# Optimization experiments

Measured on AMD Instinct MI355X. Metric: run time of the kernel, lower is better.

## Reference

```python
import jax, jax.numpy as jnp
import numpy as np

# Fixed architecture constants (match init_kwargs)
L = 4        # num_layers
E = 4        # embed_dim (forced: embedding rows are 4-bit patch vectors)
H = 512      # hidden_dim
NH = 8       # num_heads
HD = H // NH # head_dim = 64
FF = 1024    # feedforward_dim
S = 1024     # seq_len (num patches)
B = 4        # batch
NT = 17      # num_tokens (16 patterns + mask token)
MRP = 32     # max_relative_positions
EPS = 1e-5


def _layernorm(x, g, b):
    m = x.mean(-1, keepdims=True)
    v = x.var(-1, keepdims=True)  # torch LayerNorm uses biased variance
    return (x - m) / jnp.sqrt(v + EPS) * g + b


def setup_inputs() -> dict:
    key = jax.random.key(0)
    ks = jax.random.split(key, 16)
    patches = jax.random.randint(ks[0], (B, S), 0, 16)
    mask = jax.random.bernoulli(ks[1], 0.15, (B, S))
    # Frozen embedding table: rows 0..15 = binary 4-vectors, row 16 = all 2s (mask token)
    pat = np.array([[a, b, c, d] for a in range(2) for b in range(2)
                    for c in range(2) for d in range(2)], dtype=np.float32)
    emb = np.zeros((NT, E), np.float32)
    emb[:16] = pat
    emb[16] = 2.0
    emb_table = jnp.array(emb)

    def gn(k, shape, s=0.02):
        return jax.random.normal(k, shape, jnp.float32) * s

    return {
        'patches': patches,
        'mask': mask,
        'emb_table': emb_table,
        'Wi': gn(ks[2], (L, E, H)), 'bi': jnp.zeros((L, H)),
        'Wqkv': gn(ks[3], (L, H, 3 * H)), 'bqkv': jnp.zeros((L, 3 * H)),
        'Wo': gn(ks[4], (L, H, E)), 'bo': jnp.zeros((L, E)),
        'g1': jnp.ones((L, H)), 'b1n': jnp.zeros((L, H)),
        'Wf1': gn(ks[5], (L, E, FF)), 'bf1': jnp.zeros((L, FF)),
        'Wf2': gn(ks[6], (L, FF, E)), 'bf2': jnp.zeros((L, E)),
        'g2': jnp.ones((L, E)), 'b2n': jnp.zeros((L, E)),
        'relemb': jax.random.normal(ks[7], (L, 2 * MRP - 1, HD), jnp.float32),
        'Wout': gn(ks[8], (E, NT)), 'bout': jnp.zeros((NT,)),
    }


def reference(patches, mask, emb_table, Wi, bi, Wqkv, bqkv, Wo, bo,
              g1, b1n, Wf1, bf1, Wf2, bf2, g2, b2n, relemb, Wout, bout):
    # Embedding lookup + mask-token substitution
    x = emb_table[patches]                                # (B,S,E)
    x = jnp.where(mask[..., None], emb_table[-1], x)

    r = jnp.arange(S)
    relpos = jnp.clip(r[:, None] - r[None, :] + MRP - 1, 0, 2 * MRP - 2)  # (S,S)
    # The original's nested-loop mask-build reduces exactly to:
    #   score[b,q,k] += -inf  iff  mask[b,k] and q != k
    neg = jnp.where(mask[:, None, :] & (r[:, None] != r[None, :]),
                    -jnp.inf, 0.0)                        # (B,S,S)

    scale = 1.0 / np.sqrt(HD)
    for l in range(L):
        bias = relemb[l].sum(-1)[relpos]                  # (S,S) rel-pos bias
        xp = x @ Wi[l] + bi[l]                            # (B,S,H)
        xn = _layernorm(xp, g1[l], b1n[l])
        qkv = (xn @ Wqkv[l] + bqkv[l]).reshape(B, S, 3, NH, HD)
        q, k, v = qkv[:, :, 0], qkv[:, :, 1], qkv[:, :, 2]
        sc = jnp.einsum('bqhd,bkhd->bhqk', q, k) * scale + bias + neg[:, None]
        p = jax.nn.softmax(sc, axis=-1)                   # (B,NH,S,S)
        ao = jnp.einsum('bhqk,bkhd->bqhd', p, v).reshape(B, S, H)
        x = x + ao @ Wo[l] + bo[l]                        # residual 1 (embed dim E)
        ff = jax.nn.relu(_layernorm(x, g2[l], b2n[l]) @ Wf1[l] + bf1[l]) @ Wf2[l] + bf2[l]
        x = x + ff                                        # residual 2
    return x @ Wout + bout                                # (B,S,NT) logits
```

## Files before the change

### kernel.cpp

```cpp
#include <hip/hip_runtime.h>
#include <hip/hip_bf16.h>
#include <math.h>

#define B_ 4
#define S_ 1024
#define H_ 512
#define NH_ 8
#define HD_ 64
#define FF_ 1024
#define E_ 4
#define L_ 4
#define NT_ 17
#define BS_ 4096
#define EPS_ 1e-5f
#define L2E_ 1.4426950408889634f
#define SCL_ 0.18033688011112042f
#define KSPLIT_ 4

typedef __attribute__((ext_vector_type(8))) short short8;
typedef __attribute__((ext_vector_type(16))) float f32x16;
typedef float float4u __attribute__((ext_vector_type(4), aligned(4)));

__device__ inline ushort bf16_rne(float f) {
  unsigned u = __builtin_bit_cast(unsigned, f);
  u += 0x7FFFu + ((u >> 16) & 1u);
  return (ushort)(u >> 16);
}
__device__ inline unsigned pk_bf16(float a, float b) {
  return (unsigned)bf16_rne(a) | ((unsigned)bf16_rne(b) << 16);
}
__device__ inline unsigned pk2(float a, float b) {
  unsigned ua = __builtin_bit_cast(unsigned, a) + 0x8000u;
  unsigned ub = __builtin_bit_cast(unsigned, b) + 0x8000u;
  return __builtin_amdgcn_perm(ub, ua, 0x07060302u);
}
__device__ inline float ubf2f(ushort u) {
  return __builtin_bit_cast(float, ((unsigned)u) << 16);
}


__global__ __launch_bounds__(256) void k_init(const int* __restrict__ patches,
                                              const int* __restrict__ mask,
                                              const float* __restrict__ emb,
                                              const float* __restrict__ relemb,
                                              float* __restrict__ x,
                                              float* __restrict__ T,
                                              float* __restrict__ negT) {
  int gid = blockIdx.x * 256 + threadIdx.x;
  if (gid < BS_) {
    int mk = mask[gid];
    int row = mk ? (NT_ - 1) : patches[gid];
    ((float4*)x)[gid] = ((const float4*)emb)[row];
    negT[gid] = mk ? -1e30f : 0.f;
  } else {
    int idx = gid - BS_;
    if (idx < L_ * 2112) {
      int l = idx / 2112, j = idx - l * 2112;
      int c = 1086 - j;
      c = c < 0 ? 0 : (c > 62 ? 62 : c);
      const float* src = relemb + (size_t)(l * 63 + c) * 64;
      float s = 0.f;
#pragma unroll
      for (int d = 0; d < 64; d++) s += src[d];
      T[idx] = s * L2E_;
    }
  }
}

__global__ __launch_bounds__(256) void k_cvtw(const float* __restrict__ W,
                                              ushort* __restrict__ Wt) {
  __shared__ ushort Tr[64][72];
  int l = blockIdx.z, k0 = blockIdx.y * 64, n0 = blockIdx.x * 64;
  int t = threadIdx.x;
  const float* src = W + (size_t)l * 512 * 1536;
  int row = t >> 4, c4 = (t & 15) * 4;
#pragma unroll
  for (int rr = 0; rr < 4; rr++) {
    int k = rr * 16 + row;
    float4 v = *(const float4*)(src + (size_t)(k0 + k) * 1536 + n0 + c4);
    Tr[c4 + 0][k] = bf16_rne(v.x);
    Tr[c4 + 1][k] = bf16_rne(v.y);
    Tr[c4 + 2][k] = bf16_rne(v.z);
    Tr[c4 + 3][k] = bf16_rne(v.w);
  }
  __syncthreads();
  int nrow = t >> 2, kc = (t & 3) * 16;
  ushort* dst = Wt + ((size_t)(l * 1536 + n0 + nrow)) * 512 + k0 + kc;
  *(uint4*)dst = *(uint4*)&Tr[nrow][kc];
  *(uint4*)(dst + 8) = *(uint4*)&Tr[nrow][kc + 8];
}

__global__ __launch_bounds__(256) void k_inln(const float* __restrict__ x,
                                              const float* __restrict__ Wi,
                                              const float* __restrict__ bi,
                                              const float* __restrict__ g1,
                                              const float* __restrict__ b1n,
                                              ushort* __restrict__ xnbf) {
  __shared__ float red_s[4], red_q[4];
  int tok = blockIdx.x;
  int t = threadIdx.x;
  float4 xr = ((const float4*)x)[tok];
  int j0 = 2 * t, j1 = 2 * t + 1;
  float xp0 = bi[j0] + xr.x * Wi[j0] + xr.y * Wi[H_ + j0] + xr.z * Wi[2 * H_ + j0] + xr.w * Wi[3 * H_ + j0];
  float xp1 = bi[j1] + xr.x * Wi[j1] + xr.y * Wi[H_ + j1] + xr.z * Wi[2 * H_ + j1] + xr.w * Wi[3 * H_ + j1];
  float s = xp0 + xp1;
  float q = xp0 * xp0 + xp1 * xp1;
#pragma unroll
  for (int o = 32; o > 0; o >>= 1) {
    s += __shfl_xor(s, o);
    q += __shfl_xor(q, o);
  }
  int wid = t >> 6;
  if ((t & 63) == 0) { red_s[wid] = s; red_q[wid] = q; }
  __syncthreads();
  s = red_s[0] + red_s[1] + red_s[2] + red_s[3];
  q = red_q[0] + red_q[1] + red_q[2] + red_q[3];
  float mean = s * (1.f / (float)H_);
  float var = q * (1.f / (float)H_) - mean * mean;
  float rs = rsqrtf(var + EPS_);
  float v0 = (xp0 - mean) * rs * g1[j0] + b1n[j0];
  float v1 = (xp1 - mean) * rs * g1[j1] + b1n[j1];
  ((unsigned*)xnbf)[tok * 256 + t] = pk_bf16(v0, v1);
}

__global__ __launch_bounds__(256, 2) void k_qkv(const ushort* __restrict__ A,
                                                const ushort* __restrict__ Wt,
                                                const float* __restrict__ bias,
                                                ushort* __restrict__ qf,
                                                ushort* __restrict__ kf,
                                                ushort* __restrict__ vf) {
  __shared__ ushort At[2][128][72];
  __shared__ ushort Bt[2][128][72];
  int t = threadIdx.x;
  int n0 = blockIdx.x * 128, m0 = blockIdx.y * 128;
  bool tr = (n0 < 1024);
  int w = t >> 6, lq = t & 31, hh = (t >> 5) & 1;
  int wm = (w & 1) * 64, wn = (w >> 1) * 64;
  f32x16 acc[2][2];
#pragma unroll
  for (int mt = 0; mt < 2; mt++)
#pragma unroll
    for (int nt = 0; nt < 2; nt++)
#pragma unroll
      for (int i = 0; i < 16; i++) acc[mt][nt][i] = 0.f;

  uint4 ar[4], br[4];

#define QLOADREGS(k0_)                                                         \
  {                                                                            \
    _Pragma("unroll") for (int j = 0; j < 4; j++) {                            \
      int idl = 256 * j + t;                                                   \
      int row = idl >> 3, u = idl & 7;                                         \
      ar[j] = *(const uint4*)(A + (size_t)(m0 + row) * 512 + (k0_) + u * 8);   \
      br[j] = *(const uint4*)(Wt + (size_t)(n0 + row) * 512 + (k0_) + u * 8);  \
    }                                                                          \
  }
#define QWRITELDS(buf_)                                                        \
  {                                                                            \
    _Pragma("unroll") for (int j = 0; j < 4; j++) {                            \
      int idl = 256 * j + t;                                                   \
      int row = idl >> 3, u = idl & 7;                                         \
      *(uint4*)&At[buf_][row][u * 8] = ar[j];                                  \
      *(uint4*)&Bt[buf_][row][u * 8] = br[j];                                  \
    }                                                                          \
  }

  QLOADREGS(0);
  QWRITELDS(0);
  __syncthreads();

  for (int it = 0; it < 8; it++) {
    int buf = it & 1;
    if (it < 7) { QLOADREGS((it + 1) * 64); }
#pragma unroll
    for (int kc = 0; kc < 4; kc++) {
      short8 af[2], bf[2];
#pragma unroll
      for (int mt = 0; mt < 2; mt++) af[mt] = *(const short8*)&At[buf][wm + mt * 32 + lq][kc * 16 + hh * 8];
#pragma unroll
      for (int nt = 0; nt < 2; nt++) bf[nt] = *(const short8*)&Bt[buf][wn + nt * 32 + lq][kc * 16 + hh * 8];
#pragma unroll
      for (int mt = 0; mt < 2; mt++)
#pragma unroll
        for (int nt = 0; nt < 2; nt++) {
          if (tr)
            acc[mt][nt] = __builtin_amdgcn_mfma_f32_32x32x16_bf16(bf[nt], af[mt], acc[mt][nt], 0, 0, 0);
          else
            acc[mt][nt] = __builtin_amdgcn_mfma_f32_32x32x16_bf16(af[mt], bf[nt], acc[mt][nt], 0, 0, 0);
        }
    }
    if (it < 7) {
      QWRITELDS(buf ^ 1);
      __syncthreads();
    }
  }
#undef QLOADREGS
#undef QWRITELDS

  if (tr) {
#pragma unroll
    for (int mt = 0; mt < 2; mt++) {
      int token = m0 + wm + mt * 32 + lq;
      int bb = token >> 10, sr = token & 1023;
      int qt = sr >> 5, lqp = sr & 31;
#pragma unroll
      for (int nt = 0; nt < 2; nt++) {
        int nn = n0 + wn + nt * 32;
        int nloc = (nn < 512) ? nn : nn - 512;
        ushort* dst = (nn < 512) ? qf : kf;
        int hd = nloc >> 6;
        int bh = bb * 8 + hd;
        size_t fragbase = ((size_t)(bh * 32 + qt)) * 4 * 512;
#pragma unroll
        for (int rg = 0; rg < 4; rg++) {
          int nbase = nn + rg * 8 + hh * 4;
          float4 bv = *(const float4*)(bias + nbase);
          float v0 = acc[mt][nt][rg * 4 + 0] + bv.x;
          float v1 = acc[mt][nt][rg * 4 + 1] + bv.y;
          float v2 = acc[mt][nt][rg * 4 + 2] + bv.z;
          float v3 = acc[mt][nt][rg * 4 + 3] + bv.w;
          int d0 = (nloc & 63) + rg * 8 + hh * 4;
          size_t addr = fragbase + (size_t)(d0 >> 4) * 512 +
                        (size_t)(((d0 >> 3) & 1) * 32 + lqp) * 8 + (d0 & 7);
          *(uint2*)(dst + addr) = make_uint2(pk_bf16(v0, v1), pk_bf16(v2, v3));
        }
      }
    }
  } else {
#pragma unroll
    for (int nt = 0; nt < 2; nt++) {
      int n = n0 + wn + nt * 32 + lq;
      int nloc = n - 1024;
      int hd = nloc >> 6, d = nloc & 63;
      float bb_ = bias[n];
#pragma unroll
      for (int mt = 0; mt < 2; mt++) {
#pragma unroll
        for (int rg = 0; rg < 4; rg++) {
          int tb = m0 + wm + mt * 32 + rg * 8 + hh * 4;
          int bb = tb >> 10, sr = tb & 1023;
          int bh = bb * 8 + hd;
          float v0 = acc[mt][nt][rg * 4 + 0] + bb_;
          float v1 = acc[mt][nt][rg * 4 + 1] + bb_;
          float v2 = acc[mt][nt][rg * 4 + 2] + bb_;
          float v3 = acc[mt][nt][rg * 4 + 3] + bb_;
          size_t addr = ((size_t)((bh * 2 + (d >> 5)) * 64 + (sr >> 4))) * 512 +
                        (size_t)(((sr >> 3) & 1) * 32 + (d & 31)) * 8 + (sr & 7);
          *(uint2*)(vf + addr) = make_uint2(pk_bf16(v0, v1), pk_bf16(v2, v3));
        }
      }
    }
  }
}

__global__ __launch_bounds__(256, 3) void k_attn(const ushort* __restrict__ qf,
                                                 const ushort* __restrict__ kf,
                                                 const ushort* __restrict__ vf,
                                                 const float* __restrict__ Tl,
                                                 const float* __restrict__ negT,
                                                 const float* __restrict__ Wol,
                                                 float* __restrict__ AOp,
                                                 float* __restrict__ lpart) {
  __shared__ ushort Pt[4][32][72];
  int t = threadIdx.x;
  int w = t >> 6, lane = t & 63;
  int lq = lane & 31, hh = lane >> 5;
  int id = blockIdx.x;
  int bh = id & 31;
  int slot = id >> 5;
  int qtg = slot & 7, j = slot >> 3;
  int b = bh >> 3, head = bh & 7;
  int qt = qtg * 4 + w;
  int q = qt * 32 + lq;
  int kstart = j * 256;

  const ushort* qbase = qf + ((size_t)(bh * 32 + qt)) * 2048 + lane * 8;
  short8 Qf[4];
#pragma unroll
  for (int c = 0; c < 4; c++) Qf[c] = *(const short8*)(qbase + c * 512);

  float Tlo = Tl[1086];
  float Thi = Tl[1024];

  float l_run = 0.f;
  f32x16 Ot[2];
#pragma unroll
  for (int dt = 0; dt < 2; dt++)
#pragma unroll
    for (int i = 0; i < 16; i++) Ot[dt][i] = 0.f;

  for (int it = 0; it < 4; it++) {
    int k0 = kstart + it * 64;
    short8 Kb[2][4];
#pragma unroll
    for (int st = 0; st < 2; st++) {
      const ushort* kb = kf + ((size_t)(bh * 32 + (k0 >> 5) + st)) * 2048 + lane * 8;
#pragma unroll
      for (int c = 0; c < 4; c++) Kb[st][c] = *(const short8*)(kb + c * 512);
    }
    short8 Vb[2][4];
#pragma unroll
    for (int dt = 0; dt < 2; dt++) {
      const ushort* vb = vf + ((size_t)((bh * 2 + dt) * 64 + (k0 >> 4))) * 512 + lane * 8;
#pragma unroll
      for (int c = 0; c < 4; c++) Vb[dt][c] = *(const short8*)(vb + c * 512);
    }
    f32x16 sa[2];
#pragma unroll
    for (int st = 0; st < 2; st++) {
      f32x16 a;
#pragma unroll
      for (int i = 0; i < 16; i++) a[i] = 0.f;
#pragma unroll
      for (int c = 0; c < 4; c++)
        a = __builtin_amdgcn_mfma_f32_32x32x16_bf16(Kb[st][c], Qf[c], a, 0, 0, 0);
      sa[st] = a;
    }
#pragma unroll
    for (int st = 0; st < 2; st++) {
      int kt0 = k0 + st * 32;
      int delta = kt0 - qt * 32;
      if (delta >= 64 || delta <= -64) {
        float bconst = (delta >= 64) ? Tlo : Thi;
#pragma unroll
        for (int rg = 0; rg < 4; rg++) {
          int krun = kt0 + rg * 8 + hh * 4;
          float4 nv = *(const float4*)(negT + b * S_ + krun);
          float p0 = exp2f(fmaf(sa[st][rg * 4 + 0], SCL_, bconst + nv.x));
          float p1 = exp2f(fmaf(sa[st][rg * 4 + 1], SCL_, bconst + nv.y));
          float p2 = exp2f(fmaf(sa[st][rg * 4 + 2], SCL_, bconst + nv.z));
          float p3 = exp2f(fmaf(sa[st][rg * 4 + 3], SCL_, bconst + nv.w));
          l_run += (p0 + p1) + (p2 + p3);
          *(uint2*)&Pt[w][lq][st * 32 + rg * 8 + hh * 4] = make_uint2(pk2(p0, p1), pk2(p2, p3));
        }
      } else {
#pragma unroll
        for (int rg = 0; rg < 4; rg++) {
          int krun = kt0 + rg * 8 + hh * 4;
          float4u bv = *(const float4u*)(Tl + (krun - q + 31 + 1024));
          float4 nv = *(const float4*)(negT + b * S_ + krun);
          float p[4];
#pragma unroll
          for (int i = 0; i < 4; i++) {
            float nvi = (i == 0) ? nv.x : (i == 1) ? nv.y : (i == 2) ? nv.z : nv.w;
            float t0 = (krun + i == q) ? bv[i] : (bv[i] + nvi);
            p[i] = exp2f(fmaf(sa[st][rg * 4 + i], SCL_, t0));
            l_run += p[i];
          }
          *(uint2*)&Pt[w][lq][st * 32 + rg * 8 + hh * 4] = make_uint2(pk2(p[0], p[1]), pk2(p[2], p[3]));
        }
      }
    }
    short8 Pf[4];
#pragma unroll
    for (int c = 0; c < 4; c++) Pf[c] = *(const short8*)&Pt[w][lq][c * 16 + hh * 8];
#pragma unroll
    for (int dt = 0; dt < 2; dt++)
#pragma unroll
      for (int c = 0; c < 4; c++)
        Ot[dt] = __builtin_amdgcn_mfma_f32_32x32x16_bf16(Vb[dt][c], Pf[c], Ot[dt], 0, 0, 0);
  }
  const float* woh = Wol + head * 64 * 4;
  float pe0 = 0.f, pe1 = 0.f, pe2 = 0.f, pe3 = 0.f;
#pragma unroll
  for (int dt = 0; dt < 2; dt++)
#pragma unroll
    for (int rg = 0; rg < 4; rg++)
#pragma unroll
      for (int i = 0; i < 4; i++) {
        int d = dt * 32 + rg * 8 + hh * 4 + i;
        float4 wv = *(const float4*)(woh + d * 4);
        float o = Ot[dt][rg * 4 + i];
        pe0 = fmaf(o, wv.x, pe0);
        pe1 = fmaf(o, wv.y, pe1);
        pe2 = fmaf(o, wv.z, pe2);
        pe3 = fmaf(o, wv.w, pe3);
      }
  pe0 += __shfl_xor(pe0, 32);
  pe1 += __shfl_xor(pe1, 32);
  pe2 += __shfl_xor(pe2, 32);
  pe3 += __shfl_xor(pe3, 32);
  float l_tot = l_run + __shfl_xor(l_run, 32);
  if (hh == 0) {
    float* ao = AOp + (size_t)j * (BS_ * NH_ * 4) + ((size_t)(b * S_ + q) * NH_ + head) * 4;
    *(float4*)ao = make_float4(pe0, pe1, pe2, pe3);
    lpart[((size_t)j * 32 + bh) * S_ + q] = l_tot;
  }
}

__global__ __launch_bounds__(256) void k_resffn(const float* __restrict__ AOp,
                                                const float* __restrict__ lpart,
                                                const float* __restrict__ bo,
                                                const float* __restrict__ g2,
                                                const float* __restrict__ b2n,
                                                const float* __restrict__ Wf1,
                                                const float* __restrict__ bf1,
                                                const float* __restrict__ Wf2,
                                                const float* __restrict__ bf2,
                                                float* __restrict__ x,
                                                const float* __restrict__ Wi,
                                                const float* __restrict__ bi,
                                                const float* __restrict__ g1,
                                                const float* __restrict__ b1n,
                                                ushort* __restrict__ xnbf,
                                                int doinln,
                                                const float* __restrict__ Wout,
                                                const float* __restrict__ bout,
                                                float* __restrict__ out,
                                                int dofinal) {
  int tok = blockIdx.x * 4 + (threadIdx.x >> 6);
  int lane = threadIdx.x & 63;
  int b = tok >> 10, qq = tok & 1023;
  int h = lane & 7;
  int lidx = (b * 8 + h) * 1024 + qq;
  float ls = lpart[lidx] + lpart[lidx + 32768] + lpart[lidx + 65536] + lpart[lidx + 98304];
  float inv = 1.f / ls;
  size_t abase = ((size_t)tok * 8 + h) * 4;
  float4 v0 = *(const float4*)(AOp + abase);
  float4 v1 = *(const float4*)(AOp + abase + 131072);
  float4 v2 = *(const float4*)(AOp + abase + 262144);
  float4 v3 = *(const float4*)(AOp + abase + 393216);
  float r0 = (v0.x + v1.x + v2.x + v3.x) * inv;
  float r1 = (v0.y + v1.y + v2.y + v3.y) * inv;
  float r2 = (v0.z + v1.z + v2.z + v3.z) * inv;
  float r3 = (v0.w + v1.w + v2.w + v3.w) * inv;
#pragma unroll
  for (int o = 1; o < 8; o <<= 1) {
    r0 += __shfl_xor(r0, o); r1 += __shfl_xor(r1, o);
    r2 += __shfl_xor(r2, o); r3 += __shfl_xor(r3, o);
  }
  float4 xo = *(const float4*)&x[tok * 4];
  float x0 = xo.x + r0 + bo[0];
  float x1 = xo.y + r1 + bo[1];
  float x2 = xo.z + r2 + bo[2];
  float x3 = xo.w + r3 + bo[3];
  float mn = 0.25f * (x0 + x1 + x2 + x3);
  float d0 = x0 - mn, d1 = x1 - mn, d2 = x2 - mn, d3 = x3 - mn;
  float var = 0.25f * (d0 * d0 + d1 * d1 + d2 * d2 + d3 * d3);
  float rs = rsqrtf(var + EPS_);
  float l0 = d0 * rs * g2[0] + b2n[0];
  float l1 = d1 * rs * g2[1] + b2n[1];
  float l2 = d2 * rs * g2[2] + b2n[2];
  float l3 = d3 * rs * g2[3] + b2n[3];
  float f0 = 0, f1 = 0, f2 = 0, f3 = 0;
#pragma unroll
  for (int f4 = 0; f4 < FF_ / 64; f4++) {
    int f = lane + f4 * 64;
    float hh = bf1[f] + l0 * Wf1[f] + l1 * Wf1[FF_ + f] + l2 * Wf1[2 * FF_ + f] + l3 * Wf1[3 * FF_ + f];
    hh = fmaxf(hh, 0.f);
    float4 w2 = *(const float4*)&Wf2[f * 4];
    f0 += hh * w2.x; f1 += hh * w2.y; f2 += hh * w2.z; f3 += hh * w2.w;
  }
#pragma unroll
  for (int o = 1; o < 64; o <<= 1) {
    f0 += __shfl_xor(f0, o); f1 += __shfl_xor(f1, o);
    f2 += __shfl_xor(f2, o); f3 += __shfl_xor(f3, o);
  }
  x0 += f0 + bf2[0]; x1 += f1 + bf2[1]; x2 += f2 + bf2[2]; x3 += f3 + bf2[3];
  if (dofinal) {
    if (lane < NT_)
      out[tok * NT_ + lane] = bout[lane] + x0 * Wout[lane] + x1 * Wout[NT_ + lane] +
                              x2 * Wout[2 * NT_ + lane] + x3 * Wout[3 * NT_ + lane];
    return;
  }
  if (lane == 0) *(float4*)&x[tok * 4] = make_float4(x0, x1, x2, x3);
  if (doinln) {
    float xp[8];
    float s = 0.f, qs = 0.f;
#pragma unroll
    for (int k = 0; k < 8; k++) {
      int jj = 64 * k + lane;
      float v = bi[jj] + x0 * Wi[jj] + x1 * Wi[H_ + jj] + x2 * Wi[2 * H_ + jj] + x3 * Wi[3 * H_ + jj];
      xp[k] = v;
      s += v;
      qs += v * v;
    }
#pragma unroll
    for (int o = 1; o < 64; o <<= 1) {
      s += __shfl_xor(s, o);
      qs += __shfl_xor(qs, o);
    }
    float mean = s * (1.f / (float)H_);
    float var1 = qs * (1.f / (float)H_) - mean * mean;
    float rs1 = rsqrtf(var1 + EPS_);
#pragma unroll
    for (int k = 0; k < 8; k++) {
      int jj = 64 * k + lane;
      float v = (xp[k] - mean) * rs1 * g1[jj] + b1n[jj];
      xnbf[tok * H_ + jj] = bf16_rne(v);
    }
  }
}

extern "C" void kernel_launch(void* const* d_in, const int* in_sizes, int n_in,
                              void* d_out, int out_size, void* d_ws, size_t ws_size,
                              hipStream_t stream) {
  const int* patches = (const int*)d_in[0];
  const int* mask = (const int*)d_in[1];
  const float* emb = (const float*)d_in[2];
  const float* Wi = (const float*)d_in[3];
  const float* bi = (const float*)d_in[4];
  const float* Wqkv = (const float*)d_in[5];
  const float* bqkv = (const float*)d_in[6];
  const float* Wo = (const float*)d_in[7];
  const float* bo = (const float*)d_in[8];
  const float* g1 = (const float*)d_in[9];
  const float* b1n = (const float*)d_in[10];
  const float* Wf1 = (const float*)d_in[11];
  const float* bf1 = (const float*)d_in[12];
  const float* Wf2 = (const float*)d_in[13];
  const float* bf2 = (const float*)d_in[14];
  const float* g2 = (const float*)d_in[15];
  const float* b2n = (const float*)d_in[16];
  const float* relemb = (const float*)d_in[17];
  const float* Wout = (const float*)d_in[18];
  const float* bout = (const float*)d_in[19];
  float* out = (float*)d_out;

  char* p = (char*)d_ws;
  float* x = (float*)p;          p += (size_t)BS_ * 4 * 4;
  float* T = (float*)p;          p += (size_t)L_ * 2112 * 4;
  float* negT = (float*)p;       p += (size_t)BS_ * 4;
  float* AOp = (float*)p;        p += (size_t)KSPLIT_ * BS_ * NH_ * 4 * 4;
  float* lpart = (float*)p;      p += (size_t)KSPLIT_ * 32 * 1024 * 4;
  ushort* xnbf = (ushort*)p;     p += (size_t)BS_ * H_ * 2;
  ushort* Wt = (ushort*)p;       p += (size_t)L_ * 1536 * 512 * 2;
  ushort* qf = (ushort*)p;       p += (size_t)32 * 1024 * 64 * 2;
  ushort* kf = (ushort*)p;       p += (size_t)32 * 1024 * 64 * 2;
  ushort* vf = (ushort*)p;       p += (size_t)32 * 64 * 1024 * 2;

  k_init<<<dim3(49), dim3(256), 0, stream>>>(patches, mask, emb, relemb, x, T, negT);
  k_cvtw<<<dim3(24, 8, 4), dim3(256), 0, stream>>>(Wqkv, Wt);
  k_inln<<<dim3(BS_), dim3(256), 0, stream>>>(x, Wi, bi, g1, b1n, xnbf);
  for (int l = 0; l < L_; l++) {
    k_qkv<<<dim3(12, 32), dim3(256), 0, stream>>>(xnbf, Wt + (size_t)l * 1536 * 512,
                                                  bqkv + l * 3 * H_, qf, kf, vf);
    k_attn<<<dim3(1024), dim3(256), 0, stream>>>(qf, kf, vf, T + l * 2112, negT,
                                                 Wo + l * H_ * E_, AOp, lpart);
    int nl = l + 1;
    k_resffn<<<dim3(1024), dim3(256), 0, stream>>>(
        AOp, lpart, bo + l * E_, g2 + l * E_, b2n + l * E_,
        Wf1 + l * E_ * FF_, bf1 + l * FF_, Wf2 + l * FF_ * E_, bf2 + l * E_, x,
        Wi + nl * E_ * H_, bi + nl * H_, g1 + nl * H_, b1n + nl * H_, xnbf,
        (l < L_ - 1) ? 1 : 0, Wout, bout, out, (l == L_ - 1) ? 1 : 0);
  }
}
```

Measured before the change: 338.4 us.

## Fuse all layers into one persistent cooperative kernel with grid syncs

Replaces the separate init, weight-convert, input-layernorm, QKV, attention and residual/FFN launches with a single cooperative kernel of 256 blocks of 1024 threads, separated by grid.sync barriers. The QKV GEMM is re-tiled so each of 16 waves computes one 32x32 MFMA tile, and tiles are looped over the persistent blocks. The goal is to remove kernel launch overhead and inter-kernel gaps. In exchange it adds grid-wide barriers and lower occupancy from 1024-thread blocks with 72KB shared memory, and the QKV tile count (384) does not divide evenly over 256 blocks.

```diff
diff --git a/kernel.cpp b/kernel.cpp
--- a/kernel.cpp
+++ b/kernel.cpp
@@ -1,14 +1,15 @@
 #include <hip/hip_runtime.h>
+#include <hip/hip_cooperative_groups.h>
 #include <hip/hip_bf16.h>
 #include <math.h>
+
+namespace cg = cooperative_groups;
 
 #define B_ 4
 #define S_ 1024
 #define H_ 512
 #define NH_ 8
-#define HD_ 64
 #define FF_ 1024
-#define E_ 4
 #define L_ 4
 #define NT_ 17
 #define BS_ 4096
@@ -16,6 +17,7 @@
 #define L2E_ 1.4426950408889634f
 #define SCL_ 0.18033688011112042f
 #define KSPLIT_ 4
+#define SMEM_BYTES 73728
 
 typedef __attribute__((ext_vector_type(8))) short short8;
 typedef __attribute__((ext_vector_type(16))) float f32x16;
@@ -25,523 +27,440 @@
   unsigned u = __builtin_bit_cast(unsigned, f);
   u += 0x7FFFu + ((u >> 16) & 1u);
   return (ushort)(u >> 16);
-}
-__device__ inline unsigned pk_bf16(float a, float b) {
-  return (unsigned)bf16_rne(a) | ((unsigned)bf16_rne(b) << 16);
 }
 __device__ inline unsigned pk2(float a, float b) {
   unsigned ua = __builtin_bit_cast(unsigned, a) + 0x8000u;
   unsigned ub = __builtin_bit_cast(unsigned, b) + 0x8000u;
   return __builtin_amdgcn_perm(ub, ua, 0x07060302u);
 }
-__device__ inline float ubf2f(ushort u) {
-  return __builtin_bit_cast(float, ((unsigned)u) << 16);
-}
-
-
-__global__ __launch_bounds__(256) void k_init(const int* __restrict__ patches,
-                                              const int* __restrict__ mask,
-                                              const float* __restrict__ emb,
-                                              const float* __restrict__ relemb,
-                                              float* __restrict__ x,
-                                              float* __restrict__ T,
-                                              float* __restrict__ negT) {
-  int gid = blockIdx.x * 256 + threadIdx.x;
-  if (gid < BS_) {
-    int mk = mask[gid];
-    int row = mk ? (NT_ - 1) : patches[gid];
-    ((float4*)x)[gid] = ((const float4*)emb)[row];
-    negT[gid] = mk ? -1e30f : 0.f;
-  } else {
-    int idx = gid - BS_;
-    if (idx < L_ * 2112) {
-      int l = idx / 2112, j = idx - l * 2112;
-      int c = 1086 - j;
-      c = c < 0 ? 0 : (c > 62 ? 62 : c);
-      const float* src = relemb + (size_t)(l * 63 + c) * 64;
-      float s = 0.f;
-#pragma unroll
-      for (int d = 0; d < 64; d++) s += src[d];
-      T[idx] = s * L2E_;
+
+struct P_ {
+  const int *patches, *mask;
+  const float *emb, *Wi, *bi, *Wqkv, *bqkv, *Wo, *bo, *g1, *b1n;
+  const float *Wf1, *bf1, *Wf2, *bf2, *g2, *b2n, *relemb, *Wout, *bout;
+  float *out, *x, *T, *negT, *AOp, *lpart;
+  ushort *xnbf, *Wt, *qf, *kf, *vf;
+};
+
+__global__ __launch_bounds__(1024, 4) void k_all(P_ p) {
+  extern __shared__ char smem[];
+  cg::grid_group grid = cg::this_grid();
+  int bid = blockIdx.x, tid = threadIdx.x;
+  int w16 = tid >> 6, lane = tid & 63, lq = lane & 31, hh = lane >> 5;
+
+  {
+    int gid = bid * 1024 + tid;
+    if (gid < BS_) {
+      int mk = p.mask[gid];
+      int row = mk ? 16 : p.patches[gid];
+      ((float4*)p.x)[gid] = ((const float4*)p.emb)[row];
+      p.negT[gid] = mk ? -1e30f : 0.f;
+    } else {
+      int idx = gid - BS_;
+      if (idx < L_ * 2112) {
+        int l = idx / 2112, jj = idx - l * 2112;
+        int c = 1086 - jj;
+        c = c < 0 ? 0 : (c > 62 ? 62 : c);
+        const float* src = p.relemb + (size_t)(l * 63 + c) * 64;
+        float s = 0.f;
+#pragma unroll
+        for (int d = 0; d < 64; d++) s += src[d];
+        p.T[idx] = s * L2E_;
+      }
+    }
+    {
+      int token = bid * 16 + w16;
+      int mk = p.mask[token];
+      int row = mk ? 16 : p.patches[token];
+      float4 e = ((const float4*)p.emb)[row];
+      float xp[8];
+      float s = 0.f, qs = 0.f;
+#pragma unroll
+      for (int k = 0; k < 8; k++) {
+        int jj = 64 * k + lane;
+        float v = p.bi[jj] + e.x * p.Wi[jj] + e.y * p.Wi[512 + jj] +
+                  e.z * p.Wi[1024 + jj] + e.w * p.Wi[1536 + jj];
+        xp[k] = v; s += v; qs += v * v;
+      }
+#pragma unroll
+      for (int o = 1; o < 64; o <<= 1) { s += __shfl_xor(s, o); qs += __shfl_xor(qs, o); }
+      float mean = s * (1.f / 512.f);
+      float var = qs * (1.f / 512.f) - mean * mean;
+      float rs = rsqrtf(var + EPS_);
+#pragma unroll
+      for (int k = 0; k < 8; k++) {
+        int jj = 64 * k + lane;
+        p.xnbf[token * 512 + jj] = bf16_rne((xp[k] - mean) * rs * p.g1[jj] + p.b1n[jj]);
+      }
+    }
+    {
+      int q4 = tid >> 8, qtid = tid & 255;
+      int unit = bid * 4 + q4;
+      bool act = unit < 768;
+      ushort(*Tr)[72] = (ushort(*)[72])(smem + q4 * 64 * 72 * 2);
+      int l = unit / 192, rem = unit % 192;
+      int k0 = (rem / 24) * 64, n0 = (rem % 24) * 64;
+      if (act) {
+        const float* src = p.Wqkv + (size_t)l * 512 * 1536;
+        int row = qtid >> 4, c4 = (qtid & 15) * 4;
+#pragma unroll
+        for (int rr = 0; rr < 4; rr++) {
+          int k = rr * 16 + row;
+          float4 v = *(const float4*)(src + (size_t)(k0 + k) * 1536 + n0 + c4);
+          Tr[c4 + 0][k] = bf16_rne(v.x); Tr[c4 + 1][k] = bf16_rne(v.y);
+          Tr[c4 + 2][k] = bf16_rne(v.z); Tr[c4 + 3][k] = bf16_rne(v.w);
+        }
+      }
+      __syncthreads();
+      if (act) {
+        int nrow = qtid >> 2, kc = (qtid & 3) * 16;
+        ushort* dst = p.Wt + ((size_t)(l * 1536 + n0 + nrow)) * 512 + k0 + kc;
+        *(uint4*)dst = *(uint4*)&Tr[nrow][kc];
+        *(uint4*)(dst + 8) = *(uint4*)&Tr[nrow][kc + 8];
+      }
     }
   }
-}
-
-__global__ __launch_bounds__(256) void k_cvtw(const float* __restrict__ W,
-                                              ushort* __restrict__ Wt) {
-  __shared__ ushort Tr[64][72];
-  int l = blockIdx.z, k0 = blockIdx.y * 64, n0 = blockIdx.x * 64;
-  int t = threadIdx.x;
-  const float* src = W + (size_t)l * 512 * 1536;
-  int row = t >> 4, c4 = (t & 15) * 4;
-#pragma unroll
-  for (int rr = 0; rr < 4; rr++) {
-    int k = rr * 16 + row;
-    float4 v = *(const float4*)(src + (size_t)(k0 + k) * 1536 + n0 + c4);
-    Tr[c4 + 0][k] = bf16_rne(v.x);
-    Tr[c4 + 1][k] = bf16_rne(v.y);
-    Tr[c4 + 2][k] = bf16_rne(v.z);
-    Tr[c4 + 3][k] = bf16_rne(v.w);
-  }
-  __syncthreads();
-  int nrow = t >> 2, kc = (t & 3) * 16;
-  ushort* dst = Wt + ((size_t)(l * 1536 + n0 + nrow)) * 512 + k0 + kc;
-  *(uint4*)dst = *(uint4*)&Tr[nrow][kc];
-  *(uint4*)(dst + 8) = *(uint4*)&Tr[nrow][kc + 8];
-}
-
-__global__ __launch_bounds__(256) void k_inln(const float* __restrict__ x,
-                                              const float* __restrict__ Wi,
-                                              const float* __restrict__ bi,
-                                              const float* __restrict__ g1,
-                                              const float* __restrict__ b1n,
-                                              ushort* __restrict__ xnbf) {
-  __shared__ float red_s[4], red_q[4];
-  int tok = blockIdx.x;
-  int t = threadIdx.x;
-  float4 xr = ((const float4*)x)[tok];
-  int j0 = 2 * t, j1 = 2 * t + 1;
-  float xp0 = bi[j0] + xr.x * Wi[j0] + xr.y * Wi[H_ + j0] + xr.z * Wi[2 * H_ + j0] + xr.w * Wi[3 * H_ + j0];
-  float xp1 = bi[j1] + xr.x * Wi[j1] + xr.y * Wi[H_ + j1] + xr.z * Wi[2 * H_ + j1] + xr.w * Wi[3 * H_ + j1];
-  float s = xp0 + xp1;
-  float q = xp0 * xp0 + xp1 * xp1;
-#pragma unroll
-  for (int o = 32; o > 0; o >>= 1) {
-    s += __shfl_xor(s, o);
-    q += __shfl_xor(q, o);
-  }
-  int wid = t >> 6;
-  if ((t & 63) == 0) { red_s[wid] = s; red_q[wid] = q; }
-  __syncthreads();
-  s = red_s[0] + red_s[1] + red_s[2] + red_s[3];
-  q = red_q[0] + red_q[1] + red_q[2] + red_q[3];
-  float mean = s * (1.f / (float)H_);
-  float var = q * (1.f / (float)H_) - mean * mean;
-  float rs = rsqrtf(var + EPS_);
-  float v0 = (xp0 - mean) * rs * g1[j0] + b1n[j0];
-  float v1 = (xp1 - mean) * rs * g1[j1] + b1n[j1];
-  ((unsigned*)xnbf)[tok * 256 + t] = pk_bf16(v0, v1);
-}
-
-__global__ __launch_bounds__(256, 2) void k_qkv(const ushort* __restrict__ A,
-                                                const ushort* __restrict__ Wt,
-                                                const float* __restrict__ bias,
-                                                ushort* __restrict__ qf,
-                                                ushort* __restrict__ kf,
-                                                ushort* __restrict__ vf) {
-  __shared__ ushort At[2][128][72];
-  __shared__ ushort Bt[2][128][72];
-  int t = threadIdx.x;
-  int n0 = blockIdx.x * 128, m0 = blockIdx.y * 128;
-  bool tr = (n0 < 1024);
-  int w = t >> 6, lq = t & 31, hh = (t >> 5) & 1;
-  int wm = (w & 1) * 64, wn = (w >> 1) * 64;
-  f32x16 acc[2][2];
-#pragma unroll
-  for (int mt = 0; mt < 2; mt++)
-#pragma unroll
-    for (int nt = 0; nt < 2; nt++)
-#pragma unroll
-      for (int i = 0; i < 16; i++) acc[mt][nt][i] = 0.f;
-
-  uint4 ar[4], br[4];
-
-#define QLOADREGS(k0_)                                                         \
-  {                                                                            \
-    _Pragma("unroll") for (int j = 0; j < 4; j++) {                            \
-      int idl = 256 * j + t;                                                   \
-      int row = idl >> 3, u = idl & 7;                                         \
-      ar[j] = *(const uint4*)(A + (size_t)(m0 + row) * 512 + (k0_) + u * 8);   \
-      br[j] = *(const uint4*)(Wt + (size_t)(n0 + row) * 512 + (k0_) + u * 8);  \
-    }                                                                          \
-  }
-#define QWRITELDS(buf_)                                                        \
-  {                                                                            \
-    _Pragma("unroll") for (int j = 0; j < 4; j++) {                            \
-      int idl = 256 * j + t;                                                   \
-      int row = idl >> 3, u = idl & 7;                                         \
-      *(uint4*)&At[buf_][row][u * 8] = ar[j];                                  \
-      *(uint4*)&Bt[buf_][row][u * 8] = br[j];                                  \
-    }                                                                          \
-  }
-
-  QLOADREGS(0);
-  QWRITELDS(0);
-  __syncthreads();
-
-  for (int it = 0; it < 8; it++) {
-    int buf = it & 1;
-    if (it < 7) { QLOADREGS((it + 1) * 64); }
-#pragma unroll
-    for (int kc = 0; kc < 4; kc++) {
-      short8 af[2], bf[2];
-#pragma unroll
-      for (int mt = 0; mt < 2; mt++) af[mt] = *(const short8*)&At[buf][wm + mt * 32 + lq][kc * 16 + hh * 8];
-#pragma unroll
-      for (int nt = 0; nt < 2; nt++) bf[nt] = *(const short8*)&Bt[buf][wn + nt * 32 + lq][kc * 16 + hh * 8];
-#pragma unroll
-      for (int mt = 0; mt < 2; mt++)
-#pragma unroll
-        for (int nt = 0; nt < 2; nt++) {
-          if (tr)
-            acc[mt][nt] = __builtin_amdgcn_mfma_f32_32x32x16_bf16(bf[nt], af[mt], acc[mt][nt], 0, 0, 0);
-          else
-            acc[mt][nt] = __builtin_amdgcn_mfma_f32_32x32x16_bf16(af[mt], bf[nt], acc[mt][nt], 0, 0, 0);
-        }
-    }
-    if (it < 7) {
-      QWRITELDS(buf ^ 1);
-      __syncthreads();
-    }
-  }
-#undef QLOADREGS
-#undef QWRITELDS
-
-  if (tr) {
-#pragma unroll
-    for (int mt = 0; mt < 2; mt++) {
-      int token = m0 + wm + mt * 32 + lq;
-      int bb = token >> 10, sr = token & 1023;
-      int qt = sr >> 5, lqp = sr & 31;
-#pragma unroll
-      for (int nt = 0; nt < 2; nt++) {
-        int nn = n0 + wn + nt * 32;
-        int nloc = (nn < 512) ? nn : nn - 512;
-        ushort* dst = (nn < 512) ? qf : kf;
-        int hd = nloc >> 6;
-        int bh = bb * 8 + hd;
-        size_t fragbase = ((size_t)(bh * 32 + qt)) * 4 * 512;
-#pragma unroll
-        for (int rg = 0; rg < 4; rg++) {
-          int nbase = nn + rg * 8 + hh * 4;
-          float4 bv = *(const float4*)(bias + nbase);
-          float v0 = acc[mt][nt][rg * 4 + 0] + bv.x;
-          float v1 = acc[mt][nt][rg * 4 + 1] + bv.y;
-          float v2 = acc[mt][nt][rg * 4 + 2] + bv.z;
-          float v3 = acc[mt][nt][rg * 4 + 3] + bv.w;
-          int d0 = (nloc & 63) + rg * 8 + hh * 4;
-          size_t addr = fragbase + (size_t)(d0 >> 4) * 512 +
-                        (size_t)(((d0 >> 3) & 1) * 32 + lqp) * 8 + (d0 & 7);
-          *(uint2*)(dst + addr) = make_uint2(pk_bf16(v0, v1), pk_bf16(v2, v3));
-        }
-      }
-    }
-  } else {
-#pragma unroll
-    for (int nt = 0; nt < 2; nt++) {
-      int n = n0 + wn + nt * 32 + lq;
-      int nloc = n - 1024;
-      int hd = nloc >> 6, d = nloc & 63;
-      float bb_ = bias[n];
-#pragma unroll
-      for (int mt = 0; mt < 2; mt++) {
-#pragma unroll
-        for (int rg = 0; rg < 4; rg++) {
-          int tb = m0 + wm + mt * 32 + rg * 8 + hh * 4;
-          int bb = tb >> 10, sr = tb & 1023;
+  grid.sync();
+
+  for (int l = 0; l < L_; l++) {
+    {
+      const ushort* Wtl = p.Wt + (size_t)l * 1536 * 512;
+      const float* bias = p.bqkv + l * 1536;
+      ushort* Ab = (ushort*)smem;
+      ushort* Bb = Ab + 2 * 9216;
+      int wm = (w16 & 3) * 32, wn = (w16 >> 2) * 32;
+      int row = tid >> 3, u = (tid & 7) * 8;
+      for (int tidx = bid; tidx < 384; tidx += 256) {
+        int n0 = (tidx % 12) * 128, m0 = (tidx / 12) * 128;
+        bool tr = n0 < 1024;
+        f32x16 acc;
+#pragma unroll
+        for (int i = 0; i < 16; i++) acc[i] = 0.f;
+        __syncthreads();
+        uint4 ar = *(const uint4*)(p.xnbf + (size_t)(m0 + row) * 512 + u);
+        uint4 br = *(const uint4*)(Wtl + (size_t)(n0 + row) * 512 + u);
+        *(uint4*)&Ab[row * 72 + u] = ar;
+        *(uint4*)&Bb[row * 72 + u] = br;
+        __syncthreads();
+        for (int it = 0; it < 8; it++) {
+          int buf = it & 1;
+          if (it < 7) {
+            ar = *(const uint4*)(p.xnbf + (size_t)(m0 + row) * 512 + (it + 1) * 64 + u);
+            br = *(const uint4*)(Wtl + (size_t)(n0 + row) * 512 + (it + 1) * 64 + u);
+          }
+#pragma unroll
+          for (int kc = 0; kc < 4; kc++) {
+            short8 af = *(const short8*)&Ab[buf * 9216 + (wm + lq) * 72 + kc * 16 + hh * 8];
+            short8 bf = *(const short8*)&Bb[buf * 9216 + (wn + lq) * 72 + kc * 16 + hh * 8];
+            if (tr)
+              acc = __builtin_amdgcn_mfma_f32_32x32x16_bf16(bf, af, acc, 0, 0, 0);
+            else
+              acc = __builtin_amdgcn_mfma_f32_32x32x16_bf16(af, bf, acc, 0, 0, 0);
+          }
+          if (it < 7) {
+            int nb = buf ^ 1;
+            *(uint4*)&Ab[nb * 9216 + row * 72 + u] = ar;
+            *(uint4*)&Bb[nb * 9216 + row * 72 + u] = br;
+            __syncthreads();
+          }
+        }
+        if (tr) {
+          int token = m0 + wm + lq;
+          int bb = token >> 10, sr = token & 1023;
+          int qt = sr >> 5, lqp = sr & 31;
+          int nn = n0 + wn;
+          int nloc = (nn < 512) ? nn : nn - 512;
+          ushort* dst = (nn < 512) ? p.qf : p.kf;
+          int hd = nloc >> 6;
           int bh = bb * 8 + hd;
-          float v0 = acc[mt][nt][rg * 4 + 0] + bb_;
-          float v1 = acc[mt][nt][rg * 4 + 1] + bb_;
-          float v2 = acc[mt][nt][rg * 4 + 2] + bb_;
-          float v3 = acc[mt][nt][rg * 4 + 3] + bb_;
-          size_t addr = ((size_t)((bh * 2 + (d >> 5)) * 64 + (sr >> 4))) * 512 +
-                        (size_t)(((sr >> 3) & 1) * 32 + (d & 31)) * 8 + (sr & 7);
-          *(uint2*)(vf + addr) = make_uint2(pk_bf16(v0, v1), pk_bf16(v2, v3));
-        }
-      }
-    }
-  }
-}
-
-__global__ __launch_bounds__(256, 3) void k_attn(const ushort* __restrict__ qf,
-                                                 const ushort* __restrict__ kf,
-                                                 const ushort* __restrict__ vf,
-                                                 const float* __restrict__ Tl,
-                                                 const float* __restrict__ negT,
-                                                 const float* __restrict__ Wol,
-                                                 float* __restrict__ AOp,
-                                                 float* __restrict__ lpart) {
-  __shared__ ushort Pt[4][32][72];
-  int t = threadIdx.x;
-  int w = t >> 6, lane = t & 63;
-  int lq = lane & 31, hh = lane >> 5;
-  int id = blockIdx.x;
-  int bh = id & 31;
-  int slot = id >> 5;
-  int qtg = slot & 7, j = slot >> 3;
-  int b = bh >> 3, head = bh & 7;
-  int qt = qtg * 4 + w;
-  int q = qt * 32 + lq;
-  int kstart = j * 256;
-
-  const ushort* qbase = qf + ((size_t)(bh * 32 + qt)) * 2048 + lane * 8;
-  short8 Qf[4];
-#pragma unroll
-  for (int c = 0; c < 4; c++) Qf[c] = *(const short8*)(qbase + c * 512);
-
-  float Tlo = Tl[1086];
-  float Thi = Tl[1024];
-
-  float l_run = 0.f;
-  f32x16 Ot[2];
-#pragma unroll
-  for (int dt = 0; dt < 2; dt++)
-#pragma unroll
-    for (int i = 0; i < 16; i++) Ot[dt][i] = 0.f;
-
-  for (int it = 0; it < 4; it++) {
-    int k0 = kstart + it * 64;
-    short8 Kb[2][4];
-#pragma unroll
-    for (int st = 0; st < 2; st++) {
-      const ushort* kb = kf + ((size_t)(bh * 32 + (k0 >> 5) + st)) * 2048 + lane * 8;
-#pragma unroll
-      for (int c = 0; c < 4; c++) Kb[st][c] = *(const short8*)(kb + c * 512);
-    }
-    short8 Vb[2][4];
-#pragma unroll
-    for (int dt = 0; dt < 2; dt++) {
-      const ushort* vb = vf + ((size_t)((bh * 2 + dt) * 64 + (k0 >> 4))) * 512 + lane * 8;
-#pragma unroll
-      for (int c = 0; c < 4; c++) Vb[dt][c] = *(const short8*)(vb + c * 512);
-    }
-    f32x16 sa[2];
-#pragma unroll
-    for (int st = 0; st < 2; st++) {
-      f32x16 a;
-#pragma unroll
-      for (int i = 0; i < 16; i++) a[i] = 0.f;
-#pragma unroll
-      for (int c = 0; c < 4; c++)
-        a = __builtin_amdgcn_mfma_f32_32x32x16_bf16(Kb[st][c], Qf[c], a, 0, 0, 0);
-      sa[st] = a;
-    }
-#pragma unroll
-    for (int st = 0; st < 2; st++) {
-      int kt0 = k0 + st * 32;
-      int delta = kt0 - qt * 32;
-      if (delta >= 64 || delta <= -64) {
-        float bconst = (delta >= 64) ? Tlo : Thi;
-#pragma unroll
-        for (int rg = 0; rg < 4; rg++) {
-          int krun = kt0 + rg * 8 + hh * 4;
-          float4 nv = *(const float4*)(negT + b * S_ + krun);
-          float p0 = exp2f(fmaf(sa[st][rg * 4 + 0], SCL_, bconst + nv.x));
-          float p1 = exp2f(fmaf(sa[st][rg * 4 + 1], SCL_, bconst + nv.y));
-          float p2 = exp2f(fmaf(sa[st][rg * 4 + 2], SCL_, bconst + nv.z));
-          float p3 = exp2f(fmaf(sa[st][rg * 4 + 3], SCL_, bconst + nv.w));
-          l_run += (p0 + p1) + (p2 + p3);
-          *(uint2*)&Pt[w][lq][st * 32 + rg * 8 + hh * 4] = make_uint2(pk2(p0, p1), pk2(p2, p3));
-        }
+          size_t fragbase = ((size_t)(bh * 32 + qt)) * 2048;
+#pragma unroll
+          for (int rg = 0; rg < 4; rg++) {
+            int nbase = nn + rg * 8 + hh * 4;
+            float4 bv = *(const float4*)(bias + nbase);
+            float v0 = acc[rg * 4 + 0] + bv.x;
+            float v1 = acc[rg * 4 + 1] + bv.y;
+            float v2 = acc[rg * 4 + 2] + bv.z;
+            float v3 = acc[rg * 4 + 3] + bv.w;
+            int d0 = (nloc & 63) + rg * 8 + hh * 4;
+            size_t addr = fragbase + (size_t)(d0 >> 4) * 512 +
+                          (size_t)(((d0 >> 3) & 1) * 32 + lqp) * 8 + (d0 & 7);
+            *(uint2*)(dst + addr) = make_uint2(pk2(v0, v1), pk2(v2, v3));
+          }
+        } else {
+          int n = n0 + wn + lq;
+          int nloc = n - 1024;
+          int hd = nloc >> 6, d = nloc & 63;
+          float bb_ = bias[n];
+#pragma unroll
+          for (int rg = 0; rg < 4; rg++) {
+            int tb = m0 + wm + rg * 8 + hh * 4;
+            int bb = tb >> 10, sr = tb & 1023;
+            int bh = bb * 8 + hd;
+            float v0 = acc[rg * 4 + 0] + bb_;
+            float v1 = acc[rg * 4 + 1] + bb_;
+            float v2 = acc[rg * 4 + 2] + bb_;
+            float v3 = acc[rg * 4 + 3] + bb_;
+            size_t addr = ((size_t)((bh * 2 + (d >> 5)) * 64 + (sr >> 4))) * 512 +
+                          (size_t)(((sr >> 3) & 1) * 32 + (d & 31)) * 8 + (sr & 7);
+            *(uint2*)(p.vf + addr) = make_uint2(pk2(v0, v1), pk2(v2, v3));
+          }
+        }
+      }
+    }
+    grid.sync();
+
+    {
+      const float* Tl = p.T + l * 2112;
+      const float* Wol = p.Wo + l * 2048;
+      ushort* pt = (ushort*)smem + w16 * (32 * 72);
+      int u16 = w16 >> 2, w4 = w16 & 3;
+      int id = bid * 4 + u16;
+      int bh = id & 31, slot = id >> 5;
+      int qtg = slot & 7, j = slot >> 3;
+      int b = bh >> 3, head = bh & 7;
+      int qt = qtg * 4 + w4;
+      int q = qt * 32 + lq;
+      int kstart = j * 256;
+
+      const ushort* qbase = p.qf + ((size_t)(bh * 32 + qt)) * 2048 + lane * 8;
+      short8 Qf[4];
+#pragma unroll
+      for (int c = 0; c < 4; c++) Qf[c] = *(const short8*)(qbase + c * 512);
+
+      float Tlo = Tl[1086], Thi = Tl[1024];
+      float l_run = 0.f;
+      f32x16 Ot[2];
+#pragma unroll
+      for (int dt = 0; dt < 2; dt++)
+#pragma unroll
+        for (int i = 0; i < 16; i++) Ot[dt][i] = 0.f;
+
+      for (int it = 0; it < 4; it++) {
+        int k0 = kstart + it * 64;
+        short8 Kb[2][4];
+#pragma unroll
+        for (int st = 0; st < 2; st++) {
+          const ushort* kb = p.kf + ((size_t)(bh * 32 + (k0 >> 5) + st)) * 2048 + lane * 8;
+#pragma unroll
+          for (int c = 0; c < 4; c++) Kb[st][c] = *(const short8*)(kb + c * 512);
+        }
+        short8 Vb[2][4];
+#pragma unroll
+        for (int dt = 0; dt < 2; dt++) {
+          const ushort* vb = p.vf + ((size_t)((bh * 2 + dt) * 64 + (k0 >> 4))) * 512 + lane * 8;
+#pragma unroll
+          for (int c = 0; c < 4; c++) Vb[dt][c] = *(const short8*)(vb + c * 512);
+        }
+        f32x16 sa[2];
+#pragma unroll
+        for (int st = 0; st < 2; st++) {
+          f32x16 a;
+#pragma unroll
+          for (int i = 0; i < 16; i++) a[i] = 0.f;
+#pragma unroll
+          for (int c = 0; c < 4; c++)
+            a = __builtin_amdgcn_mfma_f32_32x32x16_bf16(Kb[st][c], Qf[c], a, 0, 0, 0);
+          sa[st] = a;
+        }
+#pragma unroll
+        for (int st = 0; st < 2; st++) {
+          int kt0 = k0 + st * 32;
+          int delta = kt0 - qt * 32;
+          if (delta >= 64 || delta <= -64) {
+            float bconst = (delta >= 64) ? Tlo : Thi;
+#pragma unroll
+            for (int rg = 0; rg < 4; rg++) {
+              int krun = kt0 + rg * 8 + hh * 4;
+              float4 nv = *(const float4*)(p.negT + b * S_ + krun);
+              float p0 = exp2f(fmaf(sa[st][rg * 4 + 0], SCL_, bconst + nv.x));
+              float p1 = exp2f(fmaf(sa[st][rg * 4 + 1], SCL_, bconst + nv.y));
+              float p2 = exp2f(fmaf(sa[st][rg * 4 + 2], SCL_, bconst + nv.z));
+              float p3 = exp2f(fmaf(sa[st][rg * 4 + 3], SCL_, bconst + nv.w));
+              l_run += (p0 + p1) + (p2 + p3);
+              *(uint2*)&pt[lq * 72 + st * 32 + rg * 8 + hh * 4] = make_uint2(pk2(p0, p1), pk2(p2, p3));
+            }
+          } else {
+#pragma unroll
+            for (int rg = 0; rg < 4; rg++) {
+              int krun = kt0 + rg * 8 + hh * 4;
+              float4u bv = *(const float4u*)(Tl + (krun - q + 31 + 1024));
+              float4 nv = *(const float4*)(p.negT + b * S_ + krun);
+              float pv[4];
+#pragma unroll
+              for (int i = 0; i < 4; i++) {
+                float nvi = (i == 0) ? nv.x : (i == 1) ? nv.y : (i == 2) ? nv.z : nv.w;
+                float t0 = (krun + i == q) ? bv[i] : (bv[i] + nvi);
+                pv[i] = exp2f(fmaf(sa[st][rg * 4 + i], SCL_, t0));
+                l_run += pv[i];
+              }
+              *(uint2*)&pt[lq * 72 + st * 32 + rg * 8 + hh * 4] = make_uint2(pk2(pv[0], pv[1]), pk2(pv[2], pv[3]));
+            }
+          }
+        }
+        short8 Pf[4];
+#pragma unroll
+        for (int c = 0; c < 4; c++) Pf[c] = *(const short8*)&pt[lq * 72 + c * 16 + hh * 8];
+#pragma unroll
+        for (int dt = 0; dt < 2; dt++)
+#pragma unroll
+          for (int c = 0; c < 4; c++)
+            Ot[dt] = __builtin_amdgcn_mfma_f32_32x32x16_bf16(Vb[dt][c], Pf[c], Ot[dt], 0, 0, 0);
+      }
+      const float* woh = Wol + head * 256;
+      float pe0 = 0.f, pe1 = 0.f, pe2 = 0.f, pe3 = 0.f;
+#pragma unroll
+      for (int dt = 0; dt < 2; dt++)
+#pragma unroll
+        for (int rg = 0; rg < 4; rg++)
+#pragma unroll
+          for (int i = 0; i < 4; i++) {
+            int d = dt * 32 + rg * 8 + hh * 4 + i;
+            float4 wv = *(const float4*)(woh + d * 4);
+            float o = Ot[dt][rg * 4 + i];
+            pe0 = fmaf(o, wv.x, pe0); pe1 = fmaf(o, wv.y, pe1);
+            pe2 = fmaf(o, wv.z, pe2); pe3 = fmaf(o, wv.w, pe3);
+          }
+      pe0 += __shfl_xor(pe0, 32); pe1 += __shfl_xor(pe1, 32);
+      pe2 += __shfl_xor(pe2, 32); pe3 += __shfl_xor(pe3, 32);
+      float l_tot = l_run + __shfl_xor(l_run, 32);
+      if (hh == 0) {
+        float* ao = p.AOp + (size_t)j * (BS_ * NH_ * 4) + ((size_t)(b * S_ + q) * NH_ + head) * 4;
+        *(float4*)ao = make_float4(pe0, pe1, pe2, pe3);
+        p.lpart[((size_t)j * 32 + bh) * S_ + q] = l_tot;
+      }
+    }
+    grid.sync();
+
+    {
+      int token = bid * 16 + w16;
+      int b = token >> 10, qq = token & 1023;
+      int h = lane & 7;
+      int lidx = (b * 8 + h) * 1024 + qq;
+      float ls = p.lpart[lidx] + p.lpart[lidx + 32768] + p.lpart[lidx + 65536] + p.lpart[lidx + 98304];
+      float inv = 1.f / ls;
+      size_t abase = ((size_t)token * 8 + h) * 4;
+      float4 v0 = *(const float4*)(p.AOp + abase);
+      float4 v1 = *(const float4*)(p.AOp + abase + 131072);
+      float4 v2 = *(const float4*)(p.AOp + abase + 262144);
+      float4 v3 = *(const float4*)(p.AOp + abase + 393216);
+      float r0 = (v0.x + v1.x + v2.x + v3.x) * inv;
+      float r1 = (v0.y + v1.y + v2.y + v3.y) * inv;
+      float r2 = (v0.z + v1.z + v2.z + v3.z) * inv;
+      float r3 = (v0.w + v1.w + v2.w + v3.w) * inv;
+#pragma unroll
+      for (int o = 1; o < 8; o <<= 1) {
+        r0 += __shfl_xor(r0, o); r1 += __shfl_xor(r1, o);
+        r2 += __shfl_xor(r2, o); r3 += __shfl_xor(r3, o);
+      }
+      const float* bo = p.bo + l * 4;
+      const float* g2 = p.g2 + l * 4;
+      const float* b2n = p.b2n + l * 4;
+      const float* Wf1 = p.Wf1 + l * 4096;
+      const float* bf1 = p.bf1 + l * 1024;
+      const float* Wf2 = p.Wf2 + l * 4096;
+      const float* bf2 = p.bf2 + l * 4;
+      float4 xo = *(const float4*)&p.x[token * 4];
+      float x0 = xo.x + r0 + bo[0];
+      float x1 = xo.y + r1 + bo[1];
+      float x2 = xo.z + r2 + bo[2];
+      float x3 = xo.w + r3 + bo[3];
+      float mn = 0.25f * (x0 + x1 + x2 + x3);
+      float d0 = x0 - mn, d1 = x1 - mn, d2 = x2 - mn, d3 = x3 - mn;
+      float var = 0.25f * (d0 * d0 + d1 * d1 + d2 * d2 + d3 * d3);
+      float rs = rsqrtf(var + EPS_);
+      float l0 = d0 * rs * g2[0] + b2n[0];
+      float l1 = d1 * rs * g2[1] + b2n[1];
+      float l2 = d2 * rs * g2[2] + b2n[2];
+      float l3 = d3 * rs * g2[3] + b2n[3];
+      float f0 = 0, f1 = 0, f2 = 0, f3 = 0;
+#pragma unroll
+      for (int f4 = 0; f4 < 16; f4++) {
+        int f = lane + f4 * 64;
+        float hv = bf1[f] + l0 * Wf1[f] + l1 * Wf1[1024 + f] + l2 * Wf1[2048 + f] + l3 * Wf1[3072 + f];
+        hv = fmaxf(hv, 0.f);
+        float4 w2 = *(const float4*)&Wf2[f * 4];
+        f0 += hv * w2.x; f1 += hv * w2.y; f2 += hv * w2.z; f3 += hv * w2.w;
+      }
+#pragma unroll
+      for (int o = 1; o < 64; o <<= 1) {
+        f0 += __shfl_xor(f0, o); f1 += __shfl_xor(f1, o);
+        f2 += __shfl_xor(f2, o); f3 += __shfl_xor(f3, o);
+      }
+      x0 += f0 + bf2[0]; x1 += f1 + bf2[1]; x2 += f2 + bf2[2]; x3 += f3 + bf2[3];
+      if (l == L_ - 1) {
+        if (lane < NT_)
+          p.out[token * NT_ + lane] = p.bout[lane] + x0 * p.Wout[lane] + x1 * p.Wout[NT_ + lane] +
+                                      x2 * p.Wout[2 * NT_ + lane] + x3 * p.Wout[3 * NT_ + lane];
       } else {
-#pragma unroll
-        for (int rg = 0; rg < 4; rg++) {
-          int krun = kt0 + rg * 8 + hh * 4;
-          float4u bv = *(const float4u*)(Tl + (krun - q + 31 + 1024));
-          float4 nv = *(const float4*)(negT + b * S_ + krun);
-          float p[4];
-#pragma unroll
-          for (int i = 0; i < 4; i++) {
-            float nvi = (i == 0) ? nv.x : (i == 1) ? nv.y : (i == 2) ? nv.z : nv.w;
-            float t0 = (krun + i == q) ? bv[i] : (bv[i] + nvi);
-            p[i] = exp2f(fmaf(sa[st][rg * 4 + i], SCL_, t0));
-            l_run += p[i];
-          }
-          *(uint2*)&Pt[w][lq][st * 32 + rg * 8 + hh * 4] = make_uint2(pk2(p[0], p[1]), pk2(p[2], p[3]));
-        }
-      }
-    }
-    short8 Pf[4];
-#pragma unroll
-    for (int c = 0; c < 4; c++) Pf[c] = *(const short8*)&Pt[w][lq][c * 16 + hh * 8];
-#pragma unroll
-    for (int dt = 0; dt < 2; dt++)
-#pragma unroll
-      for (int c = 0; c < 4; c++)
-        Ot[dt] = __builtin_amdgcn_mfma_f32_32x32x16_bf16(Vb[dt][c], Pf[c], Ot[dt], 0, 0, 0);
-  }
-  const float* woh = Wol + head * 64 * 4;
-  float pe0 = 0.f, pe1 = 0.f, pe2 = 0.f, pe3 = 0.f;
-#pragma unroll
-  for (int dt = 0; dt < 2; dt++)
-#pragma unroll
-    for (int rg = 0; rg < 4; rg++)
-#pragma unroll
-      for (int i = 0; i < 4; i++) {
-        int d = dt * 32 + rg * 8 + hh * 4 + i;
-        float4 wv = *(const float4*)(woh + d * 4);
-        float o = Ot[dt][rg * 4 + i];
-        pe0 = fmaf(o, wv.x, pe0);
-        pe1 = fmaf(o, wv.y, pe1);
-        pe2 = fmaf(o, wv.z, pe2);
-        pe3 = fmaf(o, wv.w, pe3);
-      }
-  pe0 += __shfl_xor(pe0, 32);
-  pe1 += __shfl_xor(pe1, 32);
-  pe2 += __shfl_xor(pe2, 32);
-  pe3 += __shfl_xor(pe3, 32);
-  float l_tot = l_run + __shfl_xor(l_run, 32);
-  if (hh == 0) {
-    float* ao = AOp + (size_t)j * (BS_ * NH_ * 4) + ((size_t)(b * S_ + q) * NH_ + head) * 4;
-    *(float4*)ao = make_float4(pe0, pe1, pe2, pe3);
-    lpart[((size_t)j * 32 + bh) * S_ + q] = l_tot;
-  }
-}
-
-__global__ __launch_bounds__(256) void k_resffn(const float* __restrict__ AOp,
-                                                const float* __restrict__ lpart,
-                                                const float* __restrict__ bo,
-                                                const float* __restrict__ g2,
-                                                const float* __restrict__ b2n,
-                                                const float* __restrict__ Wf1,
-                                                const float* __restrict__ bf1,
-                                                const float* __restrict__ Wf2,
-                                                const float* __restrict__ bf2,
-                                                float* __restrict__ x,
-                                                const float* __restrict__ Wi,
-                                                const float* __restrict__ bi,
-                                                const float* __restrict__ g1,
-                                                const float* __restrict__ b1n,
-                                                ushort* __restrict__ xnbf,
-                                                int doinln,
-                                                const float* __restrict__ Wout,
-                                                const float* __restrict__ bout,
-                                                float* __restrict__ out,
-                                                int dofinal) {
-  int tok = blockIdx.x * 4 + (threadIdx.x >> 6);
-  int lane = threadIdx.x & 63;
-  int b = tok >> 10, qq = tok & 1023;
-  int h = lane & 7;
-  int lidx = (b * 8 + h) * 1024 + qq;
-  float ls = lpart[lidx] + lpart[lidx + 32768] + lpart[lidx + 65536] + lpart[lidx + 98304];
-  float inv = 1.f / ls;
-  size_t abase = ((size_t)tok * 8 + h) * 4;
-  float4 v0 = *(const float4*)(AOp + abase);
-  float4 v1 = *(const float4*)(AOp + abase + 131072);
-  float4 v2 = *(const float4*)(AOp + abase + 262144);
-  float4 v3 = *(const float4*)(AOp + abase + 393216);
-  float r0 = (v0.x + v1.x + v2.x + v3.x) * inv;
-  float r1 = (v0.y + v1.y + v2.y + v3.y) * inv;
-  float r2 = (v0.z + v1.z + v2.z + v3.z) * inv;
-  float r3 = (v0.w + v1.w + v2.w + v3.w) * inv;
-#pragma unroll
-  for (int o = 1; o < 8; o <<= 1) {
-    r0 += __shfl_xor(r0, o); r1 += __shfl_xor(r1, o);
-    r2 += __shfl_xor(r2, o); r3 += __shfl_xor(r3, o);
-  }
-  float4 xo = *(const float4*)&x[tok * 4];
-  float x0 = xo.x + r0 + bo[0];
-  float x1 = xo.y + r1 + bo[1];
-  float x2 = xo.z + r2 + bo[2];
-  float x3 = xo.w + r3 + bo[3];
-  float mn = 0.25f * (x0 + x1 + x2 + x3);
-  float d0 = x0 - mn, d1 = x1 - mn, d2 = x2 - mn, d3 = x3 - mn;
-  float var = 0.25f * (d0 * d0 + d1 * d1 + d2 * d2 + d3 * d3);
-  float rs = rsqrtf(var + EPS_);
-  float l0 = d0 * rs * g2[0] + b2n[0];
-  float l1 = d1 * rs * g2[1] + b2n[1];
-  float l2 = d2 * rs * g2[2] + b2n[2];
-  float l3 = d3 * rs * g2[3] + b2n[3];
-  float f0 = 0, f1 = 0, f2 = 0, f3 = 0;
-#pragma unroll
-  for (int f4 = 0; f4 < FF_ / 64; f4++) {
-    int f = lane + f4 * 64;
-    float hh = bf1[f] + l0 * Wf1[f] + l1 * Wf1[FF_ + f] + l2 * Wf1[2 * FF_ + f] + l3 * Wf1[3 * FF_ + f];
-    hh = fmaxf(hh, 0.f);
-    float4 w2 = *(const float4*)&Wf2[f * 4];
-    f0 += hh * w2.x; f1 += hh * w2.y; f2 += hh * w2.z; f3 += hh * w2.w;
-  }
-#pragma unroll
-  for (int o = 1; o < 64; o <<= 1) {
-    f0 += __shfl_xor(f0, o); f1 += __shfl_xor(f1, o);
-    f2 += __shfl_xor(f2, o); f3 += __shfl_xor(f3, o);
-  }
-  x0 += f0 + bf2[0]; x1 += f1 + bf2[1]; x2 += f2 + bf2[2]; x3 += f3 + bf2[3];
-  if (dofinal) {
-    if (lane < NT_)
-      out[tok * NT_ + lane] = bout[lane] + x0 * Wout[lane] + x1 * Wout[NT_ + lane] +
-                              x2 * Wout[2 * NT_ + lane] + x3 * Wout[3 * NT_ + lane];
-    return;
-  }
-  if (lane == 0) *(float4*)&x[tok * 4] = make_float4(x0, x1, x2, x3);
-  if (doinln) {
-    float xp[8];
-    float s = 0.f, qs = 0.f;
-#pragma unroll
-    for (int k = 0; k < 8; k++) {
-      int jj = 64 * k + lane;
-      float v = bi[jj] + x0 * Wi[jj] + x1 * Wi[H_ + jj] + x2 * Wi[2 * H_ + jj] + x3 * Wi[3 * H_ + jj];
-      xp[k] = v;
-      s += v;
-      qs += v * v;
-    }
-#pragma unroll
-    for (int o = 1; o < 64; o <<= 1) {
-      s += __shfl_xor(s, o);
-      qs += __shfl_xor(qs, o);
-    }
-    float mean = s * (1.f / (float)H_);
-    float var1 = qs * (1.f / (float)H_) - mean * mean;
-    float rs1 = rsqrtf(var1 + EPS_);
-#pragma unroll
-    for (int k = 0; k < 8; k++) {
-      int jj = 64 * k + lane;
-      float v = (xp[k] - mean) * rs1 * g1[jj] + b1n[jj];
-      xnbf[tok * H_ + jj] = bf16_rne(v);
-    }
+        if (lane == 0) *(float4*)&p.x[token * 4] = make_float4(x0, x1, x2, x3);
+        const float* Wi = p.Wi + (l + 1) * 2048;
+        const float* bi = p.bi + (l + 1) * 512;
+        const float* g1 = p.g1 + (l + 1) * 512;
+        const float* b1n = p.b1n + (l + 1) * 512;
+        float xp[8];
+        float s = 0.f, qs = 0.f;
+#pragma unroll
+        for (int k = 0; k < 8; k++) {
+          int jj = 64 * k + lane;
+          float v = bi[jj] + x0 * Wi[jj] + x1 * Wi[512 + jj] + x2 * Wi[1024 + jj] + x3 * Wi[1536 + jj];
+          xp[k] = v; s += v; qs += v * v;
+        }
+#pragma unroll
+        for (int o = 1; o < 64; o <<= 1) { s += __shfl_xor(s, o); qs += __shfl_xor(qs, o); }
+        float mean = s * (1.f / 512.f);
+        float var1 = qs * (1.f / 512.f) - mean * mean;
+        float rs1 = rsqrtf(var1 + EPS_);
+#pragma unroll
+        for (int k = 0; k < 8; k++) {
+          int jj = 64 * k + lane;
+          p.xnbf[token * 512 + jj] = bf16_rne((xp[k] - mean) * rs1 * g1[jj] + b1n[jj]);
+        }
+      }
+    }
+    if (l < L_ - 1) grid.sync();
   }
 }
 
 extern "C" void kernel_launch(void* const* d_in, const int* in_sizes, int n_in,
                               void* d_out, int out_size, void* d_ws, size_t ws_size,
                               hipStream_t stream) {
-  const int* patches = (const int*)d_in[0];
-  const int* mask = (const int*)d_in[1];
-  const float* emb = (const float*)d_in[2];
-  const float* Wi = (const float*)d_in[3];
-  const float* bi = (const float*)d_in[4];
-  const float* Wqkv = (const float*)d_in[5];
-  const float* bqkv = (const float*)d_in[6];
-  const float* Wo = (const float*)d_in[7];
-  const float* bo = (const float*)d_in[8];
-  const float* g1 = (const float*)d_in[9];
-  const float* b1n = (const float*)d_in[10];
-  const float* Wf1 = (const float*)d_in[11];
-  const float* bf1 = (const float*)d_in[12];
-  const float* Wf2 = (const float*)d_in[13];
-  const float* bf2 = (const float*)d_in[14];
-  const float* g2 = (const float*)d_in[15];
-  const float* b2n = (const float*)d_in[16];
-  const float* relemb = (const float*)d_in[17];
-  const float* Wout = (const float*)d_in[18];
-  const float* bout = (const float*)d_in[19];
-  float* out = (float*)d_out;
+  P_ P;
+  P.patches = (const int*)d_in[0];
+  P.mask = (const int*)d_in[1];
+  P.emb = (const float*)d_in[2];
+  P.Wi = (const float*)d_in[3];
+  P.bi = (const float*)d_in[4];
+  P.Wqkv = (const float*)d_in[5];
+  P.bqkv = (const float*)d_in[6];
+  P.Wo = (const float*)d_in[7];
+  P.bo = (const float*)d_in[8];
+  P.g1 = (const float*)d_in[9];
+  P.b1n = (const float*)d_in[10];
+  P.Wf1 = (const float*)d_in[11];
+  P.bf1 = (const float*)d_in[12];
+  P.Wf2 = (const float*)d_in[13];
+  P.bf2 = (const float*)d_in[14];
+  P.g2 = (const float*)d_in[15];
+  P.b2n = (const float*)d_in[16];
+  P.relemb = (const float*)d_in[17];
+  P.Wout = (const float*)d_in[18];
+  P.bout = (const float*)d_in[19];
+  P.out = (float*)d_out;
 
   char* p = (char*)d_ws;
-  float* x = (float*)p;          p += (size_t)BS_ * 4 * 4;
-  float* T = (float*)p;          p += (size_t)L_ * 2112 * 4;
-  float* negT = (float*)p;       p += (size_t)BS_ * 4;
-  float* AOp = (float*)p;        p += (size_t)KSPLIT_ * BS_ * NH_ * 4 * 4;
-  float* lpart = (float*)p;      p += (size_t)KSPLIT_ * 32 * 1024 * 4;
-  ushort* xnbf = (ushort*)p;     p += (size_t)BS_ * H_ * 2;
-  ushort* Wt = (ushort*)p;       p += (size_t)L_ * 1536 * 512 * 2;
-  ushort* qf = (ushort*)p;       p += (size_t)32 * 1024 * 64 * 2;
-  ushort* kf = (ushort*)p;       p += (size_t)32 * 1024 * 64 * 2;
-  ushort* vf = (ushort*)p;       p += (size_t)32 * 64 * 1024 * 2;
-
-  k_init<<<dim3(49), dim3(256), 0, stream>>>(patches, mask, emb, relemb, x, T, negT);
-  k_cvtw<<<dim3(24, 8, 4), dim3(256), 0, stream>>>(Wqkv, Wt);
-  k_inln<<<dim3(BS_), dim3(256), 0, stream>>>(x, Wi, bi, g1, b1n, xnbf);
-  for (int l = 0; l < L_; l++) {
-    k_qkv<<<dim3(12, 32), dim3(256), 0, stream>>>(xnbf, Wt + (size_t)l * 1536 * 512,
-                                                  bqkv + l * 3 * H_, qf, kf, vf);
-    k_attn<<<dim3(1024), dim3(256), 0, stream>>>(qf, kf, vf, T + l * 2112, negT,
-                                                 Wo + l * H_ * E_, AOp, lpart);
-    int nl = l + 1;
-    k_resffn<<<dim3(1024), dim3(256), 0, stream>>>(
-        AOp, lpart, bo + l * E_, g2 + l * E_, b2n + l * E_,
-        Wf1 + l * E_ * FF_, bf1 + l * FF_, Wf2 + l * FF_ * E_, bf2 + l * E_, x,
-        Wi + nl * E_ * H_, bi + nl * H_, g1 + nl * H_, b1n + nl * H_, xnbf,
-        (l < L_ - 1) ? 1 : 0, Wout, bout, out, (l == L_ - 1) ? 1 : 0);
-  }
+  P.x = (float*)p;       p += (size_t)BS_ * 4 * 4;
+  P.T = (float*)p;       p += (size_t)L_ * 2112 * 4;
+  P.negT = (float*)p;    p += (size_t)BS_ * 4;
+  P.AOp = (float*)p;     p += (size_t)KSPLIT_ * BS_ * NH_ * 4 * 4;
+  P.lpart = (float*)p;   p += (size_t)KSPLIT_ * 32 * 1024 * 4;
+  P.xnbf = (ushort*)p;   p += (size_t)BS_ * H_ * 2;
+  P.Wt = (ushort*)p;     p += (size_t)L_ * 1536 * 512 * 2;
+  P.qf = (ushort*)p;     p += (size_t)32 * 1024 * 64 * 2;
+  P.kf = (ushort*)p;     p += (size_t)32 * 1024 * 64 * 2;
+  P.vf = (ushort*)p;     p += (size_t)32 * 64 * 1024 * 2;
+
+  void* args[] = {&P};
+  hipLaunchCooperativeKernel((const void*)k_all, dim3(256), dim3(1024), args,
+                             SMEM_BYTES, stream);
 }
```

New measurement: 816.1 us. 141% more time.
